# Kernel tuning notes

Hardware: AMD Instinct MI355X
Metric: run time of the kernel (lower is better)

## Reference

```python
import jax, jax.numpy as jnp
import numpy as np

H = W = 128          # feature-map height/width
WS = 8               # window size
SHIFT = 4            # cyclic shift (ws // 2)
HEADS = 3
C = 96               # hidden size (head_dim = 32)
MLP_FACTOR = 4
N = WS * WS          # tokens per window
NW = (H // WS) * (W // WS)  # windows per image


def _rel_pos_index():
    coords = np.stack(np.meshgrid(np.arange(WS), np.arange(WS), indexing='ij')).reshape(2, -1)
    rel = (coords[:, :, None] - coords[:, None, :]).transpose(1, 2, 0)
    rel[:, :, 0] += WS - 1
    rel[:, :, 1] += WS - 1
    rel[:, :, 0] *= 2 * WS - 1
    return rel.sum(-1)  # (N, N) int


def _window_partition_np(img):  # (H, W) -> (NW, N)
    x = img.reshape(H // WS, WS, W // WS, WS)
    return x.transpose(0, 2, 1, 3).reshape(-1, N)


def _attn_mask():
    img = np.zeros((H, W))
    cnt = 0
    sl = (slice(0, -WS), slice(-WS, -SHIFT), slice(-SHIFT, None))
    for hs in sl:
        for ws_ in sl:
            img[hs, ws_] = cnt
            cnt += 1
    win = _window_partition_np(img)
    return np.where(win[:, None, :] != win[:, :, None], -100.0, 0.0).astype(np.float32)


REL_IDX = jnp.asarray(_rel_pos_index().reshape(-1))   # (N*N,)
ATTN_MASK = jnp.asarray(_attn_mask())                 # (NW, N, N)


def _layernorm(x, g, b, eps=1e-5):
    m = x.mean(-1, keepdims=True)
    v = ((x - m) ** 2).mean(-1, keepdims=True)
    return (x - m) * jax.lax.rsqrt(v + eps) * g + b


def setup_inputs() -> dict:
    key = jax.random.key(0)
    ks = jax.random.split(key, 8)
    B = 16
    s = 0.02  # random_normal_initializer(0.0, 0.02)
    return {
        'x': jax.random.normal(ks[0], (B, H * W, C), jnp.float32),
        'ln1_g': jnp.ones((C,), jnp.float32),
        'ln1_b': jnp.zeros((C,), jnp.float32),
        'qkv_w': jax.random.normal(ks[1], (C, 3 * C), jnp.float32) * s,
        'qkv_b': jnp.zeros((3 * C,), jnp.float32),
        'proj_w': jax.random.normal(ks[2], (C, C), jnp.float32) * s,
        'bias_table': jax.random.normal(ks[3], ((2 * WS - 1) ** 2, HEADS), jnp.float32) * s,
        'ln2_g': jnp.ones((C,), jnp.float32),
        'ln2_b': jnp.zeros((C,), jnp.float32),
        'mlp_w1': jax.random.normal(ks[4], (C, MLP_FACTOR * C), jnp.float32) * s,
        'mlp_w2': jax.random.normal(ks[5], (MLP_FACTOR * C, C), jnp.float32) * s,
    }


def reference(x, ln1_g, ln1_b, qkv_w, qkv_b, proj_w, bias_table, ln2_g, ln2_b, mlp_w1, mlp_w2):
    B = x.shape[0]
    shortcut = x
    h = _layernorm(x, ln1_g, ln1_b).reshape(B, H, W, C)
    # cyclic shift
    h = jnp.roll(h, (-SHIFT, -SHIFT), axis=(1, 2))
    # window partition: (B*NW, N, C)
    h = h.reshape(B, H // WS, WS, W // WS, WS, C).transpose(0, 1, 3, 2, 4, 5).reshape(B * NW, N, C)
    # windowed MHSA
    qkv = h @ qkv_w + qkv_b
    qkv = qkv.reshape(B * NW, N, 3, HEADS, C // HEADS).transpose(2, 0, 3, 1, 4)
    q, k, v = qkv[0], qkv[1], qkv[2]
    scale = (C // HEADS) ** -0.5
    attn = jnp.einsum('whnd,whmd->whnm', q * scale, k)
    bias = bias_table[REL_IDX].reshape(N, N, HEADS).transpose(2, 0, 1)
    attn = attn + bias[None]
    attn = attn.reshape(B, NW, HEADS, N, N) + ATTN_MASK[None, :, None]
    attn = jax.nn.softmax(attn, axis=-1).reshape(B * NW, HEADS, N, N)
    out = jnp.einsum('whnm,whmd->whnd', attn, v).transpose(0, 2, 1, 3).reshape(B * NW, N, C)
    out = out @ proj_w
    # window reverse + un-shift
    out = out.reshape(B, H // WS, W // WS, WS, WS, C).transpose(0, 1, 3, 2, 4, 5).reshape(B, H, W, C)
    out = jnp.roll(out, (SHIFT, SHIFT), axis=(1, 2)).reshape(B, H * W, C)
    x = shortcut + out
    # MLP branch
    h2 = _layernorm(x, ln2_g, ln2_b)
    h2 = jax.nn.gelu(h2 @ mlp_w1) @ mlp_w2
    return x + h2
```

## Files before the change

kernel.cpp:

```cpp
#include <hip/hip_runtime.h>

#define SHIFT 4

typedef __bf16 bf16x8 __attribute__((ext_vector_type(8)));
typedef __bf16 bf16x4 __attribute__((ext_vector_type(4)));
typedef float  f32x4  __attribute__((ext_vector_type(4)));

#define LDA 104
#define LDQ 40
#define LDV 72
#define LDW 104

#define WS_W1T  36864
#define WS_W2C  73728
#define WS_BIAS_BYTES 221184

__global__ __launch_bounds__(256)
void swin_prep_kernel(const float* __restrict__ qkvw, const float* __restrict__ projw,
                      const float* __restrict__ w1, const float* __restrict__ w2,
                      const float* __restrict__ btab,
                      __bf16* __restrict__ ws)
{
  const int i = blockIdx.x * 256 + threadIdx.x;
  if (i < 36864) {
    const int fi = i >> 9, e = i & 511;
    const int lane = e >> 3, j = e & 7;
    const int l15 = lane & 15;
    const int kk  = (lane >> 4) * 8 + j;
    float v;
    if (fi < 54) {
      const int c = fi / 18, rem = fi % 18, t = rem / 3, ks = rem % 3;
      v = qkvw[(ks * 32 + kk) * 288 + c * 96 + t * 16 + l15];
    } else {
      const int f2 = fi - 54, t = f2 / 3, ks = f2 % 3;
      v = projw[(ks * 32 + kk) * 96 + t * 16 + l15];
    }
    ws[i] = (__bf16)v;
  } else if (i < 73728) {
    const int j = i - WS_W1T;
    const int col = j / 96, kk = j - col * 96;
    ws[i] = (__bf16)w1[kk * 384 + col];
  } else if (i < 110592) {
    const int j = i - WS_W2C;
    const int c = j / 9216, r2 = j - c * 9216;
    const int col = r2 / 96, kk = r2 - col * 96;
    ws[i] = (__bf16)w2[(c * 96 + kk) * 96 + col];
  } else {
    const int jj = i - 110592;
    const int h = jj >> 12, n = (jj >> 6) & 63, m = jj & 63;
    const int dy = (n >> 3) - (m >> 3), dx = (n & 7) - (m & 7);
    float* biasf = (float*)((char*)ws + WS_BIAS_BYTES);
    biasf[jj] = btab[((dy + 7) * 15 + (dx + 7)) * 3 + h];
  }
}

__global__ __launch_bounds__(256, 3)
void swin_attn_kernel(const float* __restrict__ x,
                      const float* __restrict__ ln1g, const float* __restrict__ ln1b,
                      const __bf16* __restrict__ ws, const float* __restrict__ qkvb,
                      float* __restrict__ out)
{
  __shared__ __align__(16) char lds[42496];
  __bf16* h_s = (__bf16*)lds;
  __bf16* k_s = (__bf16*)(lds + 13312);
  __bf16* v_s = (__bf16*)(lds + 28672);

  const float* biasf = (const float*)((const char*)ws + WS_BIAS_BYTES);

  const int tid  = threadIdx.x;
  const int lane = tid & 63;
  const int wv   = tid >> 6;
  const int l15  = lane & 15;
  const int g4   = lane >> 4;
  const int blk  = blockIdx.x;
  const int b    = blk >> 8;
  const int wy   = (blk >> 4) & 15;
  const int wx   = blk & 15;

  {
    const int t = tid >> 2, p = tid & 3;
    const int ti = t >> 3, tj = t & 7;
    const int iy = (wy * 8 + ti + SHIFT) & 127;
    const int ix = (wx * 8 + tj + SHIFT) & 127;
    const float* rowp = x + ((size_t)(b * 16384 + iy * 128 + ix)) * 96 + p * 24;
    float vb[24];
    float s = 0.f, ss = 0.f;
#pragma unroll
    for (int u = 0; u < 6; ++u) {
      f32x4 f = *(const f32x4*)(rowp + 4 * u);
#pragma unroll
      for (int e = 0; e < 4; ++e) { float q = f[e]; vb[4*u+e] = q; s += q; ss += q*q; }
    }
    s  += __shfl_xor(s, 1);  s  += __shfl_xor(s, 2);
    ss += __shfl_xor(ss, 1); ss += __shfl_xor(ss, 2);
    const float mean = s * (1.f / 96.f);
    const float var  = ss * (1.f / 96.f) - mean * mean;
    const float rstd = rsqrtf(var + 1e-5f);
#pragma unroll
    for (int u = 0; u < 6; ++u) {
      f32x4 gg = *(const f32x4*)(ln1g + p * 24 + 4 * u);
      f32x4 bb = *(const f32x4*)(ln1b + p * 24 + 4 * u);
      f32x4 nv;
#pragma unroll
      for (int e = 0; e < 4; ++e) nv[e] = (vb[4*u+e] - mean) * rstd * gg[e] + bb[e];
      *(bf16x4*)&h_s[t * LDA + p * 24 + 4 * u] = __builtin_convertvector(nv, bf16x4);
    }
  }

  const float qscale = 0.17677669529663687f;
  const __bf16* fbase = ws + (size_t)lane * 8;
  const int rowb = 16 * wv;
  bf16x8 aq3[3];
#pragma unroll
  for (int c = 0; c < 3; ++c) {
    bf16x8 wf[6][3];
#pragma unroll
    for (int t = 0; t < 6; ++t)
#pragma unroll
      for (int ks = 0; ks < 3; ++ks)
        wf[t][ks] = *(const bf16x8*)(fbase + (size_t)(c * 18 + t * 3 + ks) * 512);
    f32x4 acc[6];
#pragma unroll
    for (int t = 0; t < 6; ++t) {
      const float bv = qkvb[c * 96 + t * 16 + l15];
      f32x4 a4 = {bv, bv, bv, bv};
      acc[t] = a4;
    }
#pragma unroll
    for (int ks = 0; ks < 3; ++ks) {
      bf16x8 a = *(const bf16x8*)&h_s[(rowb + l15) * LDA + ks * 32 + 8 * g4];
#pragma unroll
      for (int t = 0; t < 6; ++t)
        acc[t] = __builtin_amdgcn_mfma_f32_16x16x32_bf16(a, wf[t][ks], acc[t], 0, 0, 0);
    }
    if (c == 0) {
#pragma unroll
      for (int t = 0; t < 6; ++t) {
        const int head = t >> 1, dim = (t & 1) * 16 + l15;
#pragma unroll
        for (int r = 0; r < 4; ++r)
          k_s[(head * 64 + rowb + 4 * g4 + r) * LDQ + dim] = (__bf16)(acc[t][r] * qscale);
      }
#pragma unroll
      for (int h = 0; h < 3; ++h)
        aq3[h] = *(const bf16x8*)&k_s[(h * 64 + rowb + l15) * LDQ + 8 * g4];
    } else if (c == 1) {
#pragma unroll
      for (int t = 0; t < 6; ++t) {
        const int head = t >> 1, dim = (t & 1) * 16 + l15;
#pragma unroll
        for (int r = 0; r < 4; ++r)
          k_s[(head * 64 + rowb + 4 * g4 + r) * LDQ + dim] = (__bf16)acc[t][r];
      }
    } else {
#pragma unroll
      for (int t = 0; t < 6; ++t) {
        const int head = t >> 1, dim = (t & 1) * 16 + l15;
        *(bf16x4*)&v_s[(head * 32 + dim) * LDV + rowb + 4 * g4] =
            __builtin_convertvector(acc[t], bf16x4);
      }
    }
  }

  __syncthreads();

  int qry[4], qrx[4];
#pragma unroll
  for (int r = 0; r < 4; ++r) {
    const int row = rowb + 4 * g4 + r;
    const int ti2 = row >> 3, tj2 = row & 7;
    qry[r] = (wy == 15) ? (ti2 < 4 ? 1 : 2) : 0;
    qrx[r] = (wx == 15) ? (tj2 < 4 ? 1 : 2) : 0;
  }
  const f32x4 zf = {0.f, 0.f, 0.f, 0.f};
  f32x4 ovA[3][2];
#pragma unroll
  for (int h = 0; h < 3; ++h) {
    const float* bh = biasf + h * 4096;
    float bv[4][4];
#pragma unroll
    for (int n = 0; n < 4; ++n)
#pragma unroll
      for (int r = 0; r < 4; ++r)
        bv[n][r] = bh[(rowb + 4 * g4 + r) * 64 + n * 16 + l15];

    f32x4 sc[4];
#pragma unroll
    for (int n = 0; n < 4; ++n) {
      bf16x8 bk = *(const bf16x8*)&k_s[(h * 64 + n * 16 + l15) * LDQ + 8 * g4];
      sc[n] = __builtin_amdgcn_mfma_f32_16x16x32_bf16(aq3[h], bk, zf, 0, 0, 0);
    }
#pragma unroll
    for (int n = 0; n < 4; ++n) {
      const int colt = n * 16 + l15;
      const int ki = colt >> 3, kj = colt & 7;
      const int kry = (wy == 15) ? (ki < 4 ? 1 : 2) : 0;
      const int krx = (wx == 15) ? (kj < 4 ? 1 : 2) : 0;
#pragma unroll
      for (int r = 0; r < 4; ++r) {
        const float mk = (qry[r] == kry && qrx[r] == krx) ? 0.f : -100.f;
        sc[n][r] += bv[n][r] + mk;
      }
    }
    float mx[4], sm[4];
#pragma unroll
    for (int r = 0; r < 4; ++r) {
      float m = fmaxf(fmaxf(sc[0][r], sc[1][r]), fmaxf(sc[2][r], sc[3][r]));
      m = fmaxf(m, __shfl_xor(m, 1)); m = fmaxf(m, __shfl_xor(m, 2));
      m = fmaxf(m, __shfl_xor(m, 4)); m = fmaxf(m, __shfl_xor(m, 8));
      mx[r] = m; sm[r] = 0.f;
    }
#pragma unroll
    for (int n = 0; n < 4; ++n)
#pragma unroll
      for (int r = 0; r < 4; ++r) {
        float p = __expf(sc[n][r] - mx[r]); sc[n][r] = p; sm[r] += p;
      }
#pragma unroll
    for (int r = 0; r < 4; ++r) {
      float s2 = sm[r];
      s2 += __shfl_xor(s2, 1); s2 += __shfl_xor(s2, 2);
      s2 += __shfl_xor(s2, 4); s2 += __shfl_xor(s2, 8);
      sm[r] = __builtin_amdgcn_rcpf(s2);
    }
#pragma unroll
    for (int n = 0; n < 4; ++n)
#pragma unroll
      for (int r = 0; r < 4; ++r)
        h_s[(rowb + 4 * g4 + r) * LDA + n * 16 + l15] = (__bf16)sc[n][r];
    f32x4 ov[2] = {zf, zf};
#pragma unroll
    for (int ks = 0; ks < 2; ++ks) {
      bf16x8 pa = *(const bf16x8*)&h_s[(rowb + l15) * LDA + ks * 32 + 8 * g4];
#pragma unroll
      for (int t2 = 0; t2 < 2; ++t2) {
        bf16x8 vb2 = *(const bf16x8*)&v_s[(h * 32 + t2 * 16 + l15) * LDV + ks * 32 + 8 * g4];
        ov[t2] = __builtin_amdgcn_mfma_f32_16x16x32_bf16(pa, vb2, ov[t2], 0, 0, 0);
      }
    }
#pragma unroll
    for (int t2 = 0; t2 < 2; ++t2)
#pragma unroll
      for (int r = 0; r < 4; ++r)
        ovA[h][t2][r] = ov[t2][r] * sm[r];
  }
#pragma unroll
  for (int h = 0; h < 3; ++h)
#pragma unroll
    for (int t2 = 0; t2 < 2; ++t2)
#pragma unroll
      for (int r = 0; r < 4; ++r)
        h_s[(rowb + 4 * g4 + r) * LDA + h * 32 + t2 * 16 + l15] = (__bf16)ovA[h][t2][r];

  f32x4 po[6];
#pragma unroll
  for (int t = 0; t < 6; ++t) po[t] = zf;
#pragma unroll
  for (int ks = 0; ks < 3; ++ks) {
    bf16x8 a = *(const bf16x8*)&h_s[(rowb + l15) * LDA + ks * 32 + 8 * g4];
#pragma unroll
    for (int t = 0; t < 6; ++t) {
      bf16x8 bb = *(const bf16x8*)(fbase + (size_t)(54 + t * 3 + ks) * 512);
      po[t] = __builtin_amdgcn_mfma_f32_16x16x32_bf16(a, bb, po[t], 0, 0, 0);
    }
  }
#pragma unroll
  for (int r = 0; r < 4; ++r) {
    const int row = rowb + 4 * g4 + r;
    const int ti2 = row >> 3, tj2 = row & 7;
    const int iy = (wy * 8 + ti2 + SHIFT) & 127;
    const int ix = (wx * 8 + tj2 + SHIFT) & 127;
    const size_t gbase = ((size_t)(b * 16384 + iy * 128 + ix)) * 96;
#pragma unroll
    for (int t = 0; t < 6; ++t) {
      const size_t gi = gbase + t * 16 + l15;
      out[gi] = x[gi] + po[t][r];
    }
  }
}

__global__ __launch_bounds__(512, 4)
void swin_mlp_kernel(const float* __restrict__ ln2g, const float* __restrict__ ln2b,
                     const __bf16* __restrict__ ws, float* xm)
{
  __shared__ __bf16 h_s[128][LDA];
  __shared__ __bf16 u_s[128][LDA];
  __shared__ __bf16 w_s[96][LDW];

  const int tid = threadIdx.x, lane = tid & 63, wv = tid >> 6;
  const int l15 = lane & 15, g4 = lane >> 4;
  const size_t rowg = (size_t)blockIdx.x * 128;

  {
    const int t = tid >> 2, p = tid & 3;
    const float* rowp = xm + (rowg + t) * 96 + p * 24;
    float vb[24];
    float s = 0.f, ss = 0.f;
#pragma unroll
    for (int u = 0; u < 6; ++u) {
      f32x4 f = *(const f32x4*)(rowp + 4 * u);
#pragma unroll
      for (int e = 0; e < 4; ++e) { float q = f[e]; vb[4*u+e] = q; s += q; ss += q*q; }
    }
    s  += __shfl_xor(s, 1);  s  += __shfl_xor(s, 2);
    ss += __shfl_xor(ss, 1); ss += __shfl_xor(ss, 2);
    const float mean = s * (1.f / 96.f);
    const float var  = ss * (1.f / 96.f) - mean * mean;
    const float rstd = rsqrtf(var + 1e-5f);
#pragma unroll
    for (int u = 0; u < 6; ++u) {
      f32x4 gg = *(const f32x4*)(ln2g + p * 24 + 4 * u);
      f32x4 bb = *(const f32x4*)(ln2b + p * 24 + 4 * u);
      f32x4 nv;
#pragma unroll
      for (int e = 0; e < 4; ++e) nv[e] = (vb[4*u+e] - mean) * rstd * gg[e] + bb[e];
      *(bf16x4*)&h_s[t][p * 24 + 4 * u] = __builtin_convertvector(nv, bf16x4);
    }
  }
  __syncthreads();

  const int rowb = 16 * wv;
  const f32x4 zf = {0.f, 0.f, 0.f, 0.f};
  f32x4 acc[6];
#pragma unroll
  for (int t = 0; t < 6; ++t) acc[t] = zf;

  for (int c = 0; c < 4; ++c) {
    {
      const __bf16* wsrc = ws + WS_W1T + c * 9216;
      for (int m = tid; m < 1152; m += 512) {
        const int row = m / 12, q4 = m - row * 12;
        *(uint4*)&w_s[row][q4 * 8] = *(const uint4*)&wsrc[row * 96 + q4 * 8];
      }
    }
    __syncthreads();
    f32x4 ua[6];
#pragma unroll
    for (int t = 0; t < 6; ++t) ua[t] = zf;
#pragma unroll
    for (int ks = 0; ks < 3; ++ks) {
      bf16x8 a = *(const bf16x8*)&h_s[rowb + l15][ks * 32 + 8 * g4];
#pragma unroll
      for (int t = 0; t < 6; ++t) {
        bf16x8 bb = *(const bf16x8*)&w_s[t * 16 + l15][ks * 32 + 8 * g4];
        ua[t] = __builtin_amdgcn_mfma_f32_16x16x32_bf16(a, bb, ua[t], 0, 0, 0);
      }
    }
#pragma unroll
    for (int t = 0; t < 6; ++t)
#pragma unroll
      for (int r = 0; r < 4; ++r) {
        const float v = ua[t][r];
        const float a3 = 0.7978845608028654f * (v + 0.044715f * v * v * v);
        const float e = __expf(2.f * a3);
        const float g = v - v * __builtin_amdgcn_rcpf(e + 1.f);
        u_s[rowb + 4 * g4 + r][t * 16 + l15] = (__bf16)g;
      }
    __syncthreads();
    {
      const __bf16* wsrc = ws + WS_W2C + c * 9216;
      for (int m = tid; m < 1152; m += 512) {
        const int row = m / 12, q4 = m - row * 12;
        *(uint4*)&w_s[row][q4 * 8] = *(const uint4*)&wsrc[row * 96 + q4 * 8];
      }
    }
    __syncthreads();
#pragma unroll
    for (int ks = 0; ks < 3; ++ks) {
      bf16x8 pa = *(const bf16x8*)&u_s[rowb + l15][ks * 32 + 8 * g4];
#pragma unroll
      for (int t = 0; t < 6; ++t) {
        bf16x8 bb = *(const bf16x8*)&w_s[t * 16 + l15][ks * 32 + 8 * g4];
        acc[t] = __builtin_amdgcn_mfma_f32_16x16x32_bf16(pa, bb, acc[t], 0, 0, 0);
      }
    }
    __syncthreads();
  }
#pragma unroll
  for (int r = 0; r < 4; ++r) {
    const size_t gr = (rowg + rowb + 4 * g4 + r) * 96;
#pragma unroll
    for (int t = 0; t < 6; ++t) {
      const size_t gi = gr + t * 16 + l15;
      xm[gi] = xm[gi] + acc[t][r];
    }
  }
}

extern "C" void kernel_launch(void* const* d_in, const int* in_sizes, int n_in,
                              void* d_out, int out_size, void* d_ws, size_t ws_size,
                              hipStream_t stream) {
  (void)in_sizes; (void)n_in; (void)out_size; (void)ws_size;
  const float* x     = (const float*)d_in[0];
  const float* ln1g  = (const float*)d_in[1];
  const float* ln1b  = (const float*)d_in[2];
  const float* qkvw  = (const float*)d_in[3];
  const float* qkvb  = (const float*)d_in[4];
  const float* projw = (const float*)d_in[5];
  const float* btab  = (const float*)d_in[6];
  const float* ln2g  = (const float*)d_in[7];
  const float* ln2b  = (const float*)d_in[8];
  const float* w1    = (const float*)d_in[9];
  const float* w2    = (const float*)d_in[10];
  float* out = (float*)d_out;
  __bf16* ws = (__bf16*)d_ws;

  swin_prep_kernel<<<480, 256, 0, stream>>>(qkvw, projw, w1, w2, btab, ws);
  swin_attn_kernel<<<4096, 256, 0, stream>>>(x, ln1g, ln1b, ws, qkvb, out);
  swin_mlp_kernel<<<2048, 512, 0, stream>>>(ln2g, ln2b, ws, out);
}
```

Measured before the change: 196.9 us.

## Shrink LDS footprints and retile MLP into 64-row blocks with 64-wide hidden chunks

The attention kernel now stores Q/K in a single row-major [64][LDA] buffer instead of per-head padded rows. This cuts LDS use enough to raise the launch-bounds occupancy hint from 3 to 4 blocks. The MLP kernel moves from 128-row, 512-thread blocks to 64-row, 256-thread blocks and walks the hidden dimension in six chunks of 64 instead of four of 96, with W2 re-laid out in the prep kernel to match. The aim is more concurrent blocks per CU and less LDS per block, at the cost of more weight reloads per row and more block-level syncs.

Measured after the change: 189.4 us. 3.8% less time.

```diff
diff --git a/kernel.cpp b/kernel.cpp
--- a/kernel.cpp
+++ b/kernel.cpp
@@ -5,11 +5,6 @@
 typedef __bf16 bf16x8 __attribute__((ext_vector_type(8)));
 typedef __bf16 bf16x4 __attribute__((ext_vector_type(4)));
 typedef float  f32x4  __attribute__((ext_vector_type(4)));
-
-#define LDA 104
-#define LDQ 40
-#define LDV 72
-#define LDW 104
 
 #define WS_W1T  36864
 #define WS_W2C  73728
@@ -42,9 +37,9 @@
     ws[i] = (__bf16)w1[kk * 384 + col];
   } else if (i < 110592) {
     const int j = i - WS_W2C;
-    const int c = j / 9216, r2 = j - c * 9216;
-    const int col = r2 / 96, kk = r2 - col * 96;
-    ws[i] = (__bf16)w2[(c * 96 + kk) * 96 + col];
+    const int cc = j / 6144, r2 = j - cc * 6144;
+    const int o = r2 / 64, jl = r2 - o * 64;
+    ws[i] = (__bf16)w2[(cc * 64 + jl) * 96 + o];
   } else {
     const int jj = i - 110592;
     const int h = jj >> 12, n = (jj >> 6) & 63, m = jj & 63;
@@ -54,16 +49,19 @@
   }
 }
 
-__global__ __launch_bounds__(256, 3)
+#define LDA 104
+#define LDV 72
+
+__global__ __launch_bounds__(256, 4)
 void swin_attn_kernel(const float* __restrict__ x,
                       const float* __restrict__ ln1g, const float* __restrict__ ln1b,
                       const __bf16* __restrict__ ws, const float* __restrict__ qkvb,
                       float* __restrict__ out)
 {
-  __shared__ __align__(16) char lds[42496];
+  __shared__ __align__(16) char lds[40448];
   __bf16* h_s = (__bf16*)lds;
   __bf16* k_s = (__bf16*)(lds + 13312);
-  __bf16* v_s = (__bf16*)(lds + 28672);
+  __bf16* v_s = (__bf16*)(lds + 26624);
 
   const float* biasf = (const float*)((const char*)ws + WS_BIAS_BYTES);
 
@@ -136,21 +134,21 @@
     if (c == 0) {
 #pragma unroll
       for (int t = 0; t < 6; ++t) {
-        const int head = t >> 1, dim = (t & 1) * 16 + l15;
+        const int col = (t >> 1) * 32 + (t & 1) * 16 + l15;
 #pragma unroll
         for (int r = 0; r < 4; ++r)
-          k_s[(head * 64 + rowb + 4 * g4 + r) * LDQ + dim] = (__bf16)(acc[t][r] * qscale);
+          k_s[(rowb + 4 * g4 + r) * LDA + col] = (__bf16)(acc[t][r] * qscale);
       }
 #pragma unroll
       for (int h = 0; h < 3; ++h)
-        aq3[h] = *(const bf16x8*)&k_s[(h * 64 + rowb + l15) * LDQ + 8 * g4];
+        aq3[h] = *(const bf16x8*)&k_s[(rowb + l15) * LDA + h * 32 + 8 * g4];
     } else if (c == 1) {
 #pragma unroll
       for (int t = 0; t < 6; ++t) {
-        const int head = t >> 1, dim = (t & 1) * 16 + l15;
+        const int col = (t >> 1) * 32 + (t & 1) * 16 + l15;
 #pragma unroll
         for (int r = 0; r < 4; ++r)
-          k_s[(head * 64 + rowb + 4 * g4 + r) * LDQ + dim] = (__bf16)acc[t][r];
+          k_s[(rowb + 4 * g4 + r) * LDA + col] = (__bf16)acc[t][r];
       }
     } else {
 #pragma unroll
@@ -187,7 +185,7 @@
     f32x4 sc[4];
 #pragma unroll
     for (int n = 0; n < 4; ++n) {
-      bf16x8 bk = *(const bf16x8*)&k_s[(h * 64 + n * 16 + l15) * LDQ + 8 * g4];
+      bf16x8 bk = *(const bf16x8*)&k_s[(n * 16 + l15) * LDA + h * 32 + 8 * g4];
       sc[n] = __builtin_amdgcn_mfma_f32_16x16x32_bf16(aq3[h], bk, zf, 0, 0, 0);
     }
 #pragma unroll
@@ -279,17 +277,23 @@
   }
 }
 
-__global__ __launch_bounds__(512, 4)
+#define LDH 104
+#define LDU 72
+#define LDW1 104
+#define LDW2 72
+
+__global__ __launch_bounds__(256, 4)
 void swin_mlp_kernel(const float* __restrict__ ln2g, const float* __restrict__ ln2b,
                      const __bf16* __restrict__ ws, float* xm)
 {
-  __shared__ __bf16 h_s[128][LDA];
-  __shared__ __bf16 u_s[128][LDA];
-  __shared__ __bf16 w_s[96][LDW];
+  __shared__ __align__(16) char mlds[36352];
+  __bf16* h_s = (__bf16*)mlds;
+  __bf16* u_s = (__bf16*)(mlds + 13312);
+  __bf16* w_s = (__bf16*)(mlds + 22528);
 
   const int tid = threadIdx.x, lane = tid & 63, wv = tid >> 6;
   const int l15 = lane & 15, g4 = lane >> 4;
-  const size_t rowg = (size_t)blockIdx.x * 128;
+  const size_t rowg = (size_t)blockIdx.x * 64;
 
   {
     const int t = tid >> 2, p = tid & 3;
@@ -314,7 +318,7 @@
       f32x4 nv;
 #pragma unroll
       for (int e = 0; e < 4; ++e) nv[e] = (vb[4*u+e] - mean) * rstd * gg[e] + bb[e];
-      *(bf16x4*)&h_s[t][p * 24 + 4 * u] = __builtin_convertvector(nv, bf16x4);
+      *(bf16x4*)&h_s[t * LDH + p * 24 + 4 * u] = __builtin_convertvector(nv, bf16x4);
     }
   }
   __syncthreads();
@@ -325,52 +329,53 @@
 #pragma unroll
   for (int t = 0; t < 6; ++t) acc[t] = zf;
 
-  for (int c = 0; c < 4; ++c) {
+  for (int cc = 0; cc < 6; ++cc) {
     {
-      const __bf16* wsrc = ws + WS_W1T + c * 9216;
-      for (int m = tid; m < 1152; m += 512) {
+      const __bf16* wsrc = ws + WS_W1T + cc * 6144;
+#pragma unroll
+      for (int m = tid; m < 768; m += 256) {
         const int row = m / 12, q4 = m - row * 12;
-        *(uint4*)&w_s[row][q4 * 8] = *(const uint4*)&wsrc[row * 96 + q4 * 8];
+        *(uint4*)&w_s[row * LDW1 + q4 * 8] = *(const uint4*)&wsrc[row * 96 + q4 * 8];
       }
     }
     __syncthreads();
-    f32x4 ua[6];
-#pragma unroll
-    for (int t = 0; t < 6; ++t) ua[t] = zf;
+    f32x4 ua[4];
+#pragma unroll
+    for (int t = 0; t < 4; ++t) ua[t] = zf;
 #pragma unroll
     for (int ks = 0; ks < 3; ++ks) {
-      bf16x8 a = *(const bf16x8*)&h_s[rowb + l15][ks * 32 + 8 * g4];
-#pragma unroll
-      for (int t = 0; t < 6; ++t) {
-        bf16x8 bb = *(const bf16x8*)&w_s[t * 16 + l15][ks * 32 + 8 * g4];
+      bf16x8 a = *(const bf16x8*)&h_s[(rowb + l15) * LDH + ks * 32 + 8 * g4];
+#pragma unroll
+      for (int t = 0; t < 4; ++t) {
+        bf16x8 bb = *(const bf16x8*)&w_s[(t * 16 + l15) * LDW1 + ks * 32 + 8 * g4];
         ua[t] = __builtin_amdgcn_mfma_f32_16x16x32_bf16(a, bb, ua[t], 0, 0, 0);
       }
     }
 #pragma unroll
-    for (int t = 0; t < 6; ++t)
+    for (int t = 0; t < 4; ++t)
 #pragma unroll
       for (int r = 0; r < 4; ++r) {
         const float v = ua[t][r];
-        const float a3 = 0.7978845608028654f * (v + 0.044715f * v * v * v);
-        const float e = __expf(2.f * a3);
+        const float e = __expf(1.5957691216057308f * (v + 0.044715f * v * v * v));
         const float g = v - v * __builtin_amdgcn_rcpf(e + 1.f);
-        u_s[rowb + 4 * g4 + r][t * 16 + l15] = (__bf16)g;
+        u_s[(rowb + 4 * g4 + r) * LDU + t * 16 + l15] = (__bf16)g;
       }
     __syncthreads();
     {
-      const __bf16* wsrc = ws + WS_W2C + c * 9216;
-      for (int m = tid; m < 1152; m += 512) {
-        const int row = m / 12, q4 = m - row * 12;
-        *(uint4*)&w_s[row][q4 * 8] = *(const uint4*)&wsrc[row * 96 + q4 * 8];
+      const __bf16* wsrc = ws + WS_W2C + cc * 6144;
+#pragma unroll
+      for (int m = tid; m < 768; m += 256) {
+        const int row = m >> 3, q4 = m & 7;
+        *(uint4*)&w_s[row * LDW2 + q4 * 8] = *(const uint4*)&wsrc[row * 64 + q4 * 8];
       }
     }
     __syncthreads();
 #pragma unroll
-    for (int ks = 0; ks < 3; ++ks) {
-      bf16x8 pa = *(const bf16x8*)&u_s[rowb + l15][ks * 32 + 8 * g4];
+    for (int ks = 0; ks < 2; ++ks) {
+      bf16x8 pa = *(const bf16x8*)&u_s[(rowb + l15) * LDU + ks * 32 + 8 * g4];
 #pragma unroll
       for (int t = 0; t < 6; ++t) {
-        bf16x8 bb = *(const bf16x8*)&w_s[t * 16 + l15][ks * 32 + 8 * g4];
+        bf16x8 bb = *(const bf16x8*)&w_s[(t * 16 + l15) * LDW2 + ks * 32 + 8 * g4];
         acc[t] = __builtin_amdgcn_mfma_f32_16x16x32_bf16(pa, bb, acc[t], 0, 0, 0);
       }
     }
@@ -407,5 +412,5 @@
 
   swin_prep_kernel<<<480, 256, 0, stream>>>(qkvw, projw, w1, w2, btab, ws);
   swin_attn_kernel<<<4096, 256, 0, stream>>>(x, ln1g, ln1b, ws, qkvb, out);
-  swin_mlp_kernel<<<2048, 512, 0, stream>>>(ln2g, ln2b, ws, out);
+  swin_mlp_kernel<<<4096, 256, 0, stream>>>(ln2g, ln2b, ws, out);
 }
```
